# Kernel tuning notes

Hardware: AMD Instinct MI355X
Metric: run time of the kernel (lower is better)

The kernel has to match this reference:

```python
import jax, jax.numpy as jnp
import numpy as np

N_HEADS = 32
N_KV_HEADS = 8
THETA = 10000.0


def _rope_tables(head_dim, seq_len):
    # freqs: [head_dim//2]
    freqs = 1.0 / (THETA ** (jnp.arange(0, head_dim, 2, dtype=jnp.float32) / head_dim))
    ang = jnp.arange(seq_len, dtype=jnp.float32)[:, None] * freqs[None, :]  # [T, hd/2]
    return jnp.cos(ang), jnp.sin(ang)


def _apply_rope(x, cos, sin):
    # x: [B, T, H, hd]; cos/sin: [T, hd/2] -> broadcast [1, T, 1, hd/2]
    x_even = x[..., 0::2]
    x_odd = x[..., 1::2]
    c = cos[None, :, None, :]
    s = sin[None, :, None, :]
    out_even = x_even * c - x_odd * s
    out_odd = x_even * s + x_odd * c
    # interleave back to [..., hd]
    out = jnp.stack([out_even, out_odd], axis=-1)
    return out.reshape(x.shape)


def setup_inputs() -> dict:
    key = jax.random.key(0)
    ks = jax.random.split(key, 5)
    B, T, C = 2, 2048, 2048
    kv_dim = (C // N_HEADS) * N_KV_HEADS  # 512
    sc = 1.0 / np.sqrt(C)
    return {
        "x": jax.random.normal(ks[0], (B, T, C), dtype=jnp.float32),
        "wq": jax.random.normal(ks[1], (C, C), dtype=jnp.float32) * sc,
        "wk": jax.random.normal(ks[2], (C, kv_dim), dtype=jnp.float32) * sc,
        "wv": jax.random.normal(ks[3], (C, kv_dim), dtype=jnp.float32) * sc,
        "wo": jax.random.normal(ks[4], (C, C), dtype=jnp.float32) * sc,
    }


def reference(x, wq, wk, wv, wo):
    B, T, C = x.shape
    hd = C // N_HEADS
    rep = N_HEADS // N_KV_HEADS

    q = (x @ wq).reshape(B, T, N_HEADS, hd)
    k = (x @ wk).reshape(B, T, N_KV_HEADS, hd)
    v = (x @ wv).reshape(B, T, N_KV_HEADS, hd)

    cos, sin = _rope_tables(hd, T)
    q = _apply_rope(q, cos, sin)
    k = _apply_rope(k, cos, sin)

    q = q.transpose(0, 2, 1, 3)  # [B, H, T, hd]
    k = k.transpose(0, 2, 1, 3)  # [B, KV, T, hd]
    v = v.transpose(0, 2, 1, 3)

    # GQA: repeat_interleave kv heads to match q heads
    k = jnp.repeat(k, rep, axis=1)
    v = jnp.repeat(v, rep, axis=1)

    scores = jnp.einsum("bhtd,bhsd->bhts", q, k) / jnp.sqrt(jnp.float32(hd))
    weights = jax.nn.softmax(scores, axis=-1)  # no causal mask, as in source
    out = jnp.einsum("bhts,bhsd->bhtd", weights, v)
    out = out.transpose(0, 2, 1, 3).reshape(B, T, C)
    return out @ wo
```

## Files before the change

kernel.cpp:

```cpp
#include <hip/hip_runtime.h>
#include <hip/hip_bf16.h>


typedef unsigned short u16;
typedef short bf16x8 __attribute__((ext_vector_type(8)));
typedef float f32x4 __attribute__((ext_vector_type(4)));

#define LOG2E 1.4426950408889634f
#define NFREQ (-13.287712379549449f / 32.f)

#if __has_builtin(__builtin_amdgcn_exp2f)
#define EXP2F(x) __builtin_amdgcn_exp2f(x)
#else
#define EXP2F(x) exp2f(x)
#endif

__device__ __forceinline__ float bf2f(u16 u) {
    union { unsigned v; float f; } x; x.v = ((unsigned)u) << 16; return x.f;
}
__device__ __forceinline__ u16 f2bf(float f) {
    unsigned u = __float_as_uint(f);
    u += 0x7fffu + ((u >> 16) & 1u);
    return (u16)(u >> 16);
}
__device__ __forceinline__ unsigned pack_bf16x2(float lo, float hi) {
    unsigned ul = (__float_as_uint(lo) + 0x8000u) >> 16;
    unsigned uh = (__float_as_uint(hi) + 0x8000u) & 0xffff0000u;
    return uh | ul;
}

__device__ __forceinline__ void async_copy16(const void* g, void* l) {
    __builtin_amdgcn_global_load_lds((const __attribute__((address_space(1))) void*)g,
                                     (__attribute__((address_space(3))) void*)l, 16, 0, 0);
}

__global__ void prep_kernel(const float* __restrict__ x,
                            const float* __restrict__ wq, const float* __restrict__ wk,
                            const float* __restrict__ wv, const float* __restrict__ wo,
                            u16* __restrict__ xbf, u16* __restrict__ wqkvT,
                            u16* __restrict__ woT, float2* __restrict__ rtab) {
    const int bz = blockIdx.z;
    if (bz < 4) {
        const int K = 2048;
        const float* W; u16* Wt; int N;
        switch (bz) {
            case 0:  W = wq; Wt = wqkvT;                        N = 2048; break;
            case 1:  W = wk; Wt = wqkvT + (size_t)2048 * 2048;  N = 512;  break;
            case 2:  W = wv; Wt = wqkvT + (size_t)2560 * 2048;  N = 512;  break;
            default: W = wo; Wt = woT;                          N = 2048; break;
        }
        if ((int)blockIdx.x * 32 >= N) return;
        __shared__ float tile[32][33];
        int xx = blockIdx.x * 32 + threadIdx.x;
        int y0 = blockIdx.y * 32 + threadIdx.y;
        #pragma unroll
        for (int r = 0; r < 32; r += 8)
            tile[threadIdx.y + r][threadIdx.x] = W[(size_t)(y0 + r) * N + xx];
        __syncthreads();
        int xo = blockIdx.y * 32 + threadIdx.x;
        int yo0 = blockIdx.x * 32 + threadIdx.y;
        #pragma unroll
        for (int r = 0; r < 32; r += 8)
            Wt[(size_t)(yo0 + r) * K + xo] = f2bf(tile[threadIdx.x][threadIdx.y + r]);
    } else if (bz == 4) {
        int bid = blockIdx.y * gridDim.x + blockIdx.x;
        int tid = threadIdx.y * 32 + threadIdx.x;
        const size_t n4 = (size_t)4096 * 2048 / 4;
        for (size_t i = (size_t)bid * 256 + tid; i < n4; i += (size_t)4096 * 256) {
            float4 v = ((const float4*)x)[i];
            ushort4 o;
            o.x = f2bf(v.x); o.y = f2bf(v.y); o.z = f2bf(v.z); o.w = f2bf(v.w);
            ((ushort4*)xbf)[i] = o;
        }
    } else {
        int bid = blockIdx.y * gridDim.x + blockIdx.x;
        int idx = bid * 256 + threadIdx.y * 32 + threadIdx.x;
        if (idx < 2048 * 32) {
            int t = idx >> 5, i = idx & 31;
            float freq = exp2f((float)i * NFREQ);
            float s, c;
            sincosf((float)t * freq, &s, &c);
            rtab[idx] = make_float2(c, s);
        }
    }
}

__global__ void transpose_perm_kernel(const u16* __restrict__ in, u16* __restrict__ out,
                                      int R, int C) {
    __shared__ u16 tile[32][33];
    int xx = blockIdx.x * 32 + threadIdx.x;
    int y0 = blockIdx.y * 32;
    #pragma unroll
    for (int r = threadIdx.y; r < 32; r += 8)
        tile[r][threadIdx.x] = in[(size_t)(y0 + r) * C + xx];
    __syncthreads();
    int s = y0 + threadIdx.x;
    int c = s & 63;
    int sp = (s & ~63) | (c & 32) | ((c & 15) << 1) | ((c >> 4) & 1);
    int yo = blockIdx.x * 32;
    #pragma unroll
    for (int r = threadIdx.y; r < 32; r += 8)
        out[(size_t)(yo + r) * R + sp] = tile[threadIdx.x][r];
}

__global__ __launch_bounds__(256) void gemm_qkv_kernel(const u16* __restrict__ A,
                                                       const u16* __restrict__ Bt,
                                                       u16* __restrict__ qout,
                                                       u16* __restrict__ kout,
                                                       u16* __restrict__ vout,
                                                       const float2* __restrict__ rope_tab,
                                                       int K) {
    __shared__ __align__(16) u16 As[128 * 64];
    __shared__ __align__(16) u16 Bs[128 * 64];
    const int tid = threadIdx.x;
    const int m0 = blockIdx.y * 128;
    const int n0 = blockIdx.x * 128;
    const int w = tid >> 6, lane = tid & 63;
    const int quad = lane >> 4, ln = lane & 15;
    const int wr = (w >> 1) * 64, wc = (w & 1) * 64;

    f32x4 acc[4][4];
    #pragma unroll
    for (int i = 0; i < 4; i++)
        #pragma unroll
        for (int j = 0; j < 4; j++) acc[i][j] = (f32x4){0.f, 0.f, 0.f, 0.f};

    for (int kt = 0; kt < K; kt += 64) {
        #pragma unroll
        for (int p = 0; p < 4; p++) {
            int chunk = p * 256 + tid;
            int r = chunk >> 3, cl = chunk & 7;
            int cg = cl ^ (r & 7);
            async_copy16(&A[(size_t)(m0 + r) * K + kt + cg * 8], &As[chunk * 8]);
            async_copy16(&Bt[(size_t)(n0 + r) * K + kt + cg * 8], &Bs[chunk * 8]);
        }
        __syncthreads();
        #pragma unroll
        for (int kk = 0; kk < 2; kk++) {
            bf16x8 a[4], b[4];
            #pragma unroll
            for (int i = 0; i < 4; i++) {
                int r = wr + i * 16 + ln;
                int cl = (kk * 4 + quad) ^ (ln & 7);
                a[i] = *(const bf16x8*)(&As[r * 64 + cl * 8]);
            }
            #pragma unroll
            for (int j = 0; j < 4; j++) {
                int r = wc + j * 16 + ln;
                int cl = (kk * 4 + quad) ^ (ln & 7);
                b[j] = *(const bf16x8*)(&Bs[r * 64 + cl * 8]);
            }
            #pragma unroll
            for (int i = 0; i < 4; i++)
                #pragma unroll
                for (int j = 0; j < 4; j++)
                    acc[i][j] = __builtin_amdgcn_mfma_f32_16x16x32_bf16(a[i], b[j], acc[i][j], 0, 0, 0);
        }
        __syncthreads();
    }

    int nb = n0 + wc;
    u16* dst; int ldc, coff; bool isv = false; float scale = 1.f;
    if (nb < 2048)      { dst = qout; ldc = 2048; coff = 0;    scale = 0.125f * LOG2E; }
    else if (nb < 2560) { dst = kout; ldc = 512;  coff = 2048; }
    else                { dst = vout; ldc = 512;  coff = 2560; isv = true; }

    if (isv) {
        #pragma unroll
        for (int i = 0; i < 4; i++)
            #pragma unroll
            for (int r = 0; r < 4; r++) {
                int row = m0 + wr + i * 16 + quad * 4 + r;
                #pragma unroll
                for (int j = 0; j < 4; j++)
                    dst[(size_t)row * ldc + nb + j * 16 + ln - coff] = f2bf(acc[i][j][r]);
            }
    } else {
        float fsin = (ln & 1) ? 1.f : -1.f;
        int fidx[4];
        #pragma unroll
        for (int j = 0; j < 4; j++)
            fidx[j] = ((nb + j * 16 + ln) & 63) >> 1;
        #pragma unroll
        for (int i = 0; i < 4; i++)
            #pragma unroll
            for (int r = 0; r < 4; r++) {
                int row = m0 + wr + i * 16 + quad * 4 + r;
                const float2* trow = rope_tab + (size_t)(row & 2047) * 32;
                #pragma unroll
                for (int j = 0; j < 4; j++) {
                    float v = acc[i][j][r];
                    float p = __shfl_xor(v, 1, 64);
                    float2 cs = trow[fidx[j]];
                    float rr = (v * cs.x + fsin * p * cs.y) * scale;
                    dst[(size_t)row * ldc + nb + j * 16 + ln - coff] = f2bf(rr);
                }
            }
    }
}

__global__ __launch_bounds__(256) void gemm_bt_kernel(const u16* __restrict__ A,
                                                      const u16* __restrict__ Bt,
                                                      float* __restrict__ C,
                                                      int M, int N, int K) {
    __shared__ __align__(16) u16 As[128 * 64];
    __shared__ __align__(16) u16 Bs[128 * 64];
    const int tid = threadIdx.x;
    const int m0 = blockIdx.y * 128;
    const int n0 = blockIdx.x * 128;
    const int w = tid >> 6, lane = tid & 63;
    const int quad = lane >> 4, ln = lane & 15;
    const int wr = (w >> 1) * 64, wc = (w & 1) * 64;

    f32x4 acc[4][4];
    #pragma unroll
    for (int i = 0; i < 4; i++)
        #pragma unroll
        for (int j = 0; j < 4; j++) acc[i][j] = (f32x4){0.f, 0.f, 0.f, 0.f};

    for (int kt = 0; kt < K; kt += 64) {
        #pragma unroll
        for (int p = 0; p < 4; p++) {
            int chunk = p * 256 + tid;
            int r = chunk >> 3, cl = chunk & 7;
            int cg = cl ^ (r & 7);
            async_copy16(&A[(size_t)(m0 + r) * K + kt + cg * 8], &As[chunk * 8]);
            async_copy16(&Bt[(size_t)(n0 + r) * K + kt + cg * 8], &Bs[chunk * 8]);
        }
        __syncthreads();
        #pragma unroll
        for (int kk = 0; kk < 2; kk++) {
            bf16x8 a[4], b[4];
            #pragma unroll
            for (int i = 0; i < 4; i++) {
                int r = wr + i * 16 + ln;
                int cl = (kk * 4 + quad) ^ (ln & 7);
                a[i] = *(const bf16x8*)(&As[r * 64 + cl * 8]);
            }
            #pragma unroll
            for (int j = 0; j < 4; j++) {
                int r = wc + j * 16 + ln;
                int cl = (kk * 4 + quad) ^ (ln & 7);
                b[j] = *(const bf16x8*)(&Bs[r * 64 + cl * 8]);
            }
            #pragma unroll
            for (int i = 0; i < 4; i++)
                #pragma unroll
                for (int j = 0; j < 4; j++)
                    acc[i][j] = __builtin_amdgcn_mfma_f32_16x16x32_bf16(a[i], b[j], acc[i][j], 0, 0, 0);
        }
        __syncthreads();
    }
    #pragma unroll
    for (int i = 0; i < 4; i++)
        #pragma unroll
        for (int r = 0; r < 4; r++) {
            int row = m0 + wr + i * 16 + quad * 4 + r;
            #pragma unroll
            for (int j = 0; j < 4; j++)
                C[(size_t)row * N + n0 + wc + j * 16 + ln] = acc[i][j][r];
        }
}

__global__ __launch_bounds__(256) void attn_kernel(const u16* __restrict__ qb,
                                                   const u16* __restrict__ kb,
                                                   const u16* __restrict__ vtb,
                                                   u16* __restrict__ ob) {
    const int T = 2048;
    const int CQ = 2048, CKV = 512;
    __shared__ __align__(16) u16 Ks[128 * 64];
    __shared__ __align__(16) u16 Vt[64 * 128];
    __shared__ __align__(16) u16 Ps[4 * 32 * 72];

    const int tid = threadIdx.x;
    const int bh = blockIdx.y;
    const int b = bh >> 5, h = bh & 31, kvh = h >> 2;
    const int t0 = blockIdx.x * 128;
    const u16* qbase = qb + ((size_t)(b * T + t0) * CQ + h * 64);
    const u16* kbase = kb + ((size_t)(b * T) * CKV + kvh * 64);
    const u16* vtbase = vtb + ((size_t)(kvh * 64)) * 4096 + b * 2048;

    const int w = tid >> 6, lane = tid & 63, quad = lane >> 4, ln = lane & 15;
    u16* Pw = &Ps[w * 32 * 72];

    bf16x8 ones;
    #pragma unroll
    for (int e = 0; e < 8; e++) ones[e] = (short)0x3F80;

    bf16x8 qf[2][2];
    #pragma unroll
    for (int i = 0; i < 2; i++)
        #pragma unroll
        for (int kk = 0; kk < 2; kk++)
            qf[i][kk] = *(const bf16x8*)(&qbase[(size_t)(w * 32 + i * 16 + ln) * CQ + kk * 32 + quad * 8]);

    f32x4 o_acc[2][4];
    f32x4 l_acc[2];
    #pragma unroll
    for (int i = 0; i < 2; i++) {
        l_acc[i] = (f32x4){0.f, 0.f, 0.f, 0.f};
        #pragma unroll
        for (int j = 0; j < 4; j++) o_acc[i][j] = (f32x4){0.f, 0.f, 0.f, 0.f};
    }

    for (int st = 0; st < T; st += 128) {
        #pragma unroll
        for (int p = 0; p < 4; p++) {
            int chunk = p * 256 + tid;
            int r = chunk >> 3, cl = chunk & 7;
            int cg = cl ^ (r & 7);
            async_copy16(&kbase[(size_t)(st + r) * CKV + cg * 8], &Ks[chunk * 8]);
            int d = chunk >> 4, cl2 = chunk & 15;
            int cg2 = cl2 ^ (d & 7);
            async_copy16(&vtbase[(size_t)d * 4096 + st + cg2 * 8], &Vt[chunk * 8]);
        }
        __syncthreads();

        f32x4 s_acc[2][8];
        #pragma unroll
        for (int i = 0; i < 2; i++)
            #pragma unroll
            for (int j = 0; j < 8; j++) s_acc[i][j] = (f32x4){0.f, 0.f, 0.f, 0.f};
        #pragma unroll
        for (int kk = 0; kk < 2; kk++) {
            bf16x8 bfr[8];
            #pragma unroll
            for (int j = 0; j < 8; j++) {
                int r = j * 16 + ln;
                int cl = (kk * 4 + quad) ^ (ln & 7);
                bfr[j] = *(const bf16x8*)(&Ks[r * 64 + cl * 8]);
            }
            #pragma unroll
            for (int i = 0; i < 2; i++)
                #pragma unroll
                for (int j = 0; j < 8; j++)
                    s_acc[i][j] = __builtin_amdgcn_mfma_f32_16x16x32_bf16(qf[i][kk], bfr[j], s_acc[i][j], 0, 0, 0);
        }

        #pragma unroll
        for (int h2 = 0; h2 < 2; h2++) {
            #pragma unroll
            for (int i = 0; i < 2; i++)
                #pragma unroll
                for (int rr = 0; rr < 4; rr++) {
                    int row = i * 16 + quad * 4 + rr;
                    unsigned* prow = (unsigned*)&Pw[row * 72];
                    float v0 = EXP2F(s_acc[i][h2 * 4 + 0][rr]);
                    float v1 = EXP2F(s_acc[i][h2 * 4 + 1][rr]);
                    float v2 = EXP2F(s_acc[i][h2 * 4 + 2][rr]);
                    float v3 = EXP2F(s_acc[i][h2 * 4 + 3][rr]);
                    prow[ln]      = pack_bf16x2(v0, v1);
                    prow[16 + ln] = pack_bf16x2(v2, v3);
                }
            #pragma unroll
            for (int kk = 0; kk < 2; kk++) {
                bf16x8 pa[2], vb[4];
                #pragma unroll
                for (int i = 0; i < 2; i++)
                    pa[i] = *(const bf16x8*)(&Pw[(i * 16 + ln) * 72 + kk * 32 + quad * 8]);
                #pragma unroll
                for (int jd = 0; jd < 4; jd++) {
                    int d = jd * 16 + ln;
                    int cg = h2 * 8 + kk * 4 + quad;
                    int cl = (cg & 8) | ((cg ^ (d & 7)) & 7);
                    vb[jd] = *(const bf16x8*)(&Vt[d * 128 + cl * 8]);
                }
                #pragma unroll
                for (int i = 0; i < 2; i++) {
                    l_acc[i] = __builtin_amdgcn_mfma_f32_16x16x32_bf16(pa[i], ones, l_acc[i], 0, 0, 0);
                    #pragma unroll
                    for (int jd = 0; jd < 4; jd++)
                        o_acc[i][jd] = __builtin_amdgcn_mfma_f32_16x16x32_bf16(pa[i], vb[jd], o_acc[i][jd], 0, 0, 0);
                }
            }
        }
        __syncthreads();
    }

    #pragma unroll
    for (int i = 0; i < 2; i++)
        #pragma unroll
        for (int rr = 0; rr < 4; rr++) {
            float linv = 1.f / l_acc[i][rr];
            int row = w * 32 + i * 16 + quad * 4 + rr;
            #pragma unroll
            for (int jd = 0; jd < 4; jd++) {
                int col = jd * 16 + ln;
                ob[(size_t)(b * T + t0 + row) * CQ + h * 64 + col] = f2bf(o_acc[i][jd][rr] * linv);
            }
        }
}

#define WS_X_BF   ((size_t)0)
#define WS_WQKVT  ((size_t)16777216)
#define WS_WOT    ((size_t)29360128)
#define WS_QBF    ((size_t)37748736)
#define WS_KBF    ((size_t)54525952)
#define WS_VBF    ((size_t)58720256)
#define WS_ABF    ((size_t)62914560)

extern "C" void kernel_launch(void* const* d_in, const int* in_sizes, int n_in,
                              void* d_out, int out_size, void* d_ws, size_t ws_size,
                              hipStream_t stream) {
    const float* x  = (const float*)d_in[0];
    const float* wq = (const float*)d_in[1];
    const float* wk = (const float*)d_in[2];
    const float* wv = (const float*)d_in[3];
    const float* wo = (const float*)d_in[4];
    char* ws = (char*)d_ws;
    u16* xbf   = (u16*)(ws + WS_X_BF);
    u16* wqkvT = (u16*)(ws + WS_WQKVT);
    u16* woT   = (u16*)(ws + WS_WOT);
    u16* qbf   = (u16*)(ws + WS_QBF);
    u16* kbf   = (u16*)(ws + WS_KBF);
    u16* vbf   = (u16*)(ws + WS_VBF);
    u16* vtbf  = (u16*)(ws + WS_X_BF);
    u16* abf   = (u16*)(ws + WS_ABF);
    float2* rtab = (float2*)(ws + WS_ABF);
    float* out = (float*)d_out;

    prep_kernel<<<dim3(64, 64, 6), dim3(32, 8), 0, stream>>>(x, wq, wk, wv, wo,
                                                             xbf, wqkvT, woT, rtab);

    gemm_qkv_kernel<<<dim3(24, 32), 256, 0, stream>>>(xbf, wqkvT, qbf, kbf, vbf, rtab, 2048);

    transpose_perm_kernel<<<dim3(16, 128), dim3(32, 8), 0, stream>>>(vbf, vtbf, 4096, 512);

    attn_kernel<<<dim3(16, 64), 256, 0, stream>>>(qbf, kbf, vtbf, abf);

    gemm_bt_kernel<<<dim3(16, 32), 256, 0, stream>>>(abf, woT, out, 4096, 2048, 2048);
}
```

Before: 338.4 us.

## Load K and V fragments directly from global memory in attention kernel

Removes the shared-memory staging of K and V tiles and the per-tile barriers. Each wave now reads its MFMA operand fragments straight from global memory (via L1/L2), and the kernel declares a minimum of four blocks per multiprocessor. The aim is to drop LDS traffic and synchronisation and to raise occupancy. In exchange, all four waves load the same K/V data redundantly, and global load latency is exposed without an explicit prefetch.

New measurement: 576.2 us. 70.3% more time.

```diff
diff --git a/kernel.cpp b/kernel.cpp
--- a/kernel.cpp
+++ b/kernel.cpp
@@ -262,14 +262,12 @@
         }
 }
 
-__global__ __launch_bounds__(256) void attn_kernel(const u16* __restrict__ qb,
-                                                   const u16* __restrict__ kb,
-                                                   const u16* __restrict__ vtb,
-                                                   u16* __restrict__ ob) {
+__global__ __launch_bounds__(256, 4) void attn_kernel(const u16* __restrict__ qb,
+                                                      const u16* __restrict__ kb,
+                                                      const u16* __restrict__ vtb,
+                                                      u16* __restrict__ ob) {
     const int T = 2048;
     const int CQ = 2048, CKV = 512;
-    __shared__ __align__(16) u16 Ks[128 * 64];
-    __shared__ __align__(16) u16 Vt[64 * 128];
     __shared__ __align__(16) u16 Ps[4 * 32 * 72];
 
     const int tid = threadIdx.x;
@@ -287,6 +285,9 @@
     #pragma unroll
     for (int e = 0; e < 8; e++) ones[e] = (short)0x3F80;
 
+    const u16* klane = kbase + (size_t)ln * CKV + quad * 8;
+    const u16* vlane = vtbase + (size_t)ln * 4096 + quad * 8;
+
     bf16x8 qf[2][2];
     #pragma unroll
     for (int i = 0; i < 2; i++)
@@ -304,18 +305,6 @@
     }
 
     for (int st = 0; st < T; st += 128) {
-        #pragma unroll
-        for (int p = 0; p < 4; p++) {
-            int chunk = p * 256 + tid;
-            int r = chunk >> 3, cl = chunk & 7;
-            int cg = cl ^ (r & 7);
-            async_copy16(&kbase[(size_t)(st + r) * CKV + cg * 8], &Ks[chunk * 8]);
-            int d = chunk >> 4, cl2 = chunk & 15;
-            int cg2 = cl2 ^ (d & 7);
-            async_copy16(&vtbase[(size_t)d * 4096 + st + cg2 * 8], &Vt[chunk * 8]);
-        }
-        __syncthreads();
-
         f32x4 s_acc[2][8];
         #pragma unroll
         for (int i = 0; i < 2; i++)
@@ -325,11 +314,8 @@
         for (int kk = 0; kk < 2; kk++) {
             bf16x8 bfr[8];
             #pragma unroll
-            for (int j = 0; j < 8; j++) {
-                int r = j * 16 + ln;
-                int cl = (kk * 4 + quad) ^ (ln & 7);
-                bfr[j] = *(const bf16x8*)(&Ks[r * 64 + cl * 8]);
-            }
+            for (int j = 0; j < 8; j++)
+                bfr[j] = *(const bf16x8*)(klane + (size_t)(st + j * 16) * CKV + kk * 32);
             #pragma unroll
             for (int i = 0; i < 2; i++)
                 #pragma unroll
@@ -359,12 +345,8 @@
                 for (int i = 0; i < 2; i++)
                     pa[i] = *(const bf16x8*)(&Pw[(i * 16 + ln) * 72 + kk * 32 + quad * 8]);
                 #pragma unroll
-                for (int jd = 0; jd < 4; jd++) {
-                    int d = jd * 16 + ln;
-                    int cg = h2 * 8 + kk * 4 + quad;
-                    int cl = (cg & 8) | ((cg ^ (d & 7)) & 7);
-                    vb[jd] = *(const bf16x8*)(&Vt[d * 128 + cl * 8]);
-                }
+                for (int jd = 0; jd < 4; jd++)
+                    vb[jd] = *(const bf16x8*)(vlane + (size_t)(jd * 16) * 4096 + st + h2 * 64 + kk * 32);
                 #pragma unroll
                 for (int i = 0; i < 2; i++) {
                     l_acc[i] = __builtin_amdgcn_mfma_f32_16x16x32_bf16(pa[i], ones, l_acc[i], 0, 0, 0);
@@ -374,7 +356,6 @@
                 }
             }
         }
-        __syncthreads();
     }
 
     #pragma unroll
```

## Keep softmax probabilities in registers by computing S^T and permuting V layout

Applied to the files above, without the earlier changes.

The attention kernel now computes the transposed score tile (K as the A operand, Q as B), so each lane's MFMA outputs line up with the A-operand layout needed for the P·V product. The probabilities are packed into bf16x8 fragments straight from registers, and the per-wave shared-memory P buffer with its write/read round trip is removed. To match this, the V transpose kernel uses a new 128-wide column permutation. The change also precomputes the K/V async-copy pointers once and advances them per tile, and wraps the MFMA bursts with s_setprio. The cost is extra register pressure from holding pa[2][4], and correctness depends on the new permutation matching the fragment ordering exactly.

After: 327.9 us. 3.1% less time.

```diff
diff --git a/kernel.cpp b/kernel.cpp
--- a/kernel.cpp
+++ b/kernel.cpp
@@ -5,6 +5,7 @@
 typedef unsigned short u16;
 typedef short bf16x8 __attribute__((ext_vector_type(8)));
 typedef float f32x4 __attribute__((ext_vector_type(4)));
+typedef unsigned uint32x4 __attribute__((ext_vector_type(4)));
 
 #define LOG2E 1.4426950408889634f
 #define NFREQ (-13.287712379549449f / 32.f)
@@ -95,8 +96,8 @@
         tile[r][threadIdx.x] = in[(size_t)(y0 + r) * C + xx];
     __syncthreads();
     int s = y0 + threadIdx.x;
-    int c = s & 63;
-    int sp = (s & ~63) | (c & 32) | ((c & 15) << 1) | ((c >> 4) & 1);
+    int c = s & 127;
+    int sp = (s & ~127) | (c & 96) | ((c & 12) << 1) | ((c & 16) >> 2) | (c & 3);
     int yo = blockIdx.x * 32;
     #pragma unroll
     for (int r = threadIdx.y; r < 32; r += 8)
@@ -270,7 +271,6 @@
     const int CQ = 2048, CKV = 512;
     __shared__ __align__(16) u16 Ks[128 * 64];
     __shared__ __align__(16) u16 Vt[64 * 128];
-    __shared__ __align__(16) u16 Ps[4 * 32 * 72];
 
     const int tid = threadIdx.x;
     const int bh = blockIdx.y;
@@ -281,11 +281,22 @@
     const u16* vtbase = vtb + ((size_t)(kvh * 64)) * 4096 + b * 2048;
 
     const int w = tid >> 6, lane = tid & 63, quad = lane >> 4, ln = lane & 15;
-    u16* Pw = &Ps[w * 32 * 72];
 
     bf16x8 ones;
     #pragma unroll
     for (int e = 0; e < 8; e++) ones[e] = (short)0x3F80;
+
+    const u16* kp[4]; const u16* vp[4];
+    #pragma unroll
+    for (int p = 0; p < 4; p++) {
+        int chunk = p * 256 + tid;
+        int r = chunk >> 3, cl = chunk & 7;
+        int cg = cl ^ (r & 7);
+        kp[p] = kbase + (size_t)r * CKV + cg * 8;
+        int d = chunk >> 4, cl2 = chunk & 15;
+        int cg2 = cl2 ^ (d & 7);
+        vp[p] = vtbase + (size_t)d * 4096 + cg2 * 8;
+    }
 
     bf16x8 qf[2][2];
     #pragma unroll
@@ -307,72 +318,69 @@
         #pragma unroll
         for (int p = 0; p < 4; p++) {
             int chunk = p * 256 + tid;
-            int r = chunk >> 3, cl = chunk & 7;
-            int cg = cl ^ (r & 7);
-            async_copy16(&kbase[(size_t)(st + r) * CKV + cg * 8], &Ks[chunk * 8]);
-            int d = chunk >> 4, cl2 = chunk & 15;
-            int cg2 = cl2 ^ (d & 7);
-            async_copy16(&vtbase[(size_t)d * 4096 + st + cg2 * 8], &Vt[chunk * 8]);
-        }
-        __syncthreads();
-
-        f32x4 s_acc[2][8];
-        #pragma unroll
-        for (int i = 0; i < 2; i++)
-            #pragma unroll
-            for (int j = 0; j < 8; j++) s_acc[i][j] = (f32x4){0.f, 0.f, 0.f, 0.f};
+            async_copy16(kp[p], &Ks[chunk * 8]);
+            async_copy16(vp[p], &Vt[chunk * 8]);
+            kp[p] += 128 * CKV;
+            vp[p] += 128;
+        }
+        __syncthreads();
+
+        f32x4 s_acc[8][2];
+        #pragma unroll
+        for (int j = 0; j < 8; j++)
+            #pragma unroll
+            for (int i = 0; i < 2; i++) s_acc[j][i] = (f32x4){0.f, 0.f, 0.f, 0.f};
         #pragma unroll
         for (int kk = 0; kk < 2; kk++) {
-            bf16x8 bfr[8];
+            bf16x8 kf[8];
             #pragma unroll
             for (int j = 0; j < 8; j++) {
                 int r = j * 16 + ln;
                 int cl = (kk * 4 + quad) ^ (ln & 7);
-                bfr[j] = *(const bf16x8*)(&Ks[r * 64 + cl * 8]);
-            }
-            #pragma unroll
-            for (int i = 0; i < 2; i++)
-                #pragma unroll
-                for (int j = 0; j < 8; j++)
-                    s_acc[i][j] = __builtin_amdgcn_mfma_f32_16x16x32_bf16(qf[i][kk], bfr[j], s_acc[i][j], 0, 0, 0);
-        }
-
-        #pragma unroll
-        for (int h2 = 0; h2 < 2; h2++) {
-            #pragma unroll
-            for (int i = 0; i < 2; i++)
-                #pragma unroll
-                for (int rr = 0; rr < 4; rr++) {
-                    int row = i * 16 + quad * 4 + rr;
-                    unsigned* prow = (unsigned*)&Pw[row * 72];
-                    float v0 = EXP2F(s_acc[i][h2 * 4 + 0][rr]);
-                    float v1 = EXP2F(s_acc[i][h2 * 4 + 1][rr]);
-                    float v2 = EXP2F(s_acc[i][h2 * 4 + 2][rr]);
-                    float v3 = EXP2F(s_acc[i][h2 * 4 + 3][rr]);
-                    prow[ln]      = pack_bf16x2(v0, v1);
-                    prow[16 + ln] = pack_bf16x2(v2, v3);
-                }
-            #pragma unroll
-            for (int kk = 0; kk < 2; kk++) {
-                bf16x8 pa[2], vb[4];
+                kf[j] = *(const bf16x8*)(&Ks[r * 64 + cl * 8]);
+            }
+            __builtin_amdgcn_s_setprio(1);
+            #pragma unroll
+            for (int j = 0; j < 8; j++)
                 #pragma unroll
                 for (int i = 0; i < 2; i++)
-                    pa[i] = *(const bf16x8*)(&Pw[(i * 16 + ln) * 72 + kk * 32 + quad * 8]);
-                #pragma unroll
-                for (int jd = 0; jd < 4; jd++) {
-                    int d = jd * 16 + ln;
-                    int cg = h2 * 8 + kk * 4 + quad;
-                    int cl = (cg & 8) | ((cg ^ (d & 7)) & 7);
-                    vb[jd] = *(const bf16x8*)(&Vt[d * 128 + cl * 8]);
-                }
-                #pragma unroll
-                for (int i = 0; i < 2; i++) {
-                    l_acc[i] = __builtin_amdgcn_mfma_f32_16x16x32_bf16(pa[i], ones, l_acc[i], 0, 0, 0);
-                    #pragma unroll
-                    for (int jd = 0; jd < 4; jd++)
-                        o_acc[i][jd] = __builtin_amdgcn_mfma_f32_16x16x32_bf16(pa[i], vb[jd], o_acc[i][jd], 0, 0, 0);
-                }
-            }
+                    s_acc[j][i] = __builtin_amdgcn_mfma_f32_16x16x32_bf16(kf[j], qf[i][kk], s_acc[j][i], 0, 0, 0);
+            __builtin_amdgcn_s_setprio(0);
+        }
+
+        bf16x8 pa[2][4];
+        #pragma unroll
+        for (int i = 0; i < 2; i++)
+            #pragma unroll
+            for (int c = 0; c < 4; c++) {
+                unsigned w0 = pack_bf16x2(EXP2F(s_acc[2 * c][i][0]),     EXP2F(s_acc[2 * c][i][1]));
+                unsigned w1 = pack_bf16x2(EXP2F(s_acc[2 * c][i][2]),     EXP2F(s_acc[2 * c][i][3]));
+                unsigned w2 = pack_bf16x2(EXP2F(s_acc[2 * c + 1][i][0]), EXP2F(s_acc[2 * c + 1][i][1]));
+                unsigned w3 = pack_bf16x2(EXP2F(s_acc[2 * c + 1][i][2]), EXP2F(s_acc[2 * c + 1][i][3]));
+                union { uint32x4 u; bf16x8 b; } pu;
+                pu.u = (uint32x4){w0, w1, w2, w3};
+                pa[i][c] = pu.b;
+            }
+
+        #pragma unroll
+        for (int c = 0; c < 4; c++) {
+            bf16x8 vb[4];
+            #pragma unroll
+            for (int jd = 0; jd < 4; jd++) {
+                int d = jd * 16 + ln;
+                int cg = c * 4 + quad;
+                int cl = (cg & 8) | ((cg ^ (d & 7)) & 7);
+                vb[jd] = *(const bf16x8*)(&Vt[d * 128 + cl * 8]);
+            }
+            __builtin_amdgcn_s_setprio(1);
+            #pragma unroll
+            for (int i = 0; i < 2; i++) {
+                l_acc[i] = __builtin_amdgcn_mfma_f32_16x16x32_bf16(pa[i][c], ones, l_acc[i], 0, 0, 0);
+                #pragma unroll
+                for (int jd = 0; jd < 4; jd++)
+                    o_acc[i][jd] = __builtin_amdgcn_mfma_f32_16x16x32_bf16(pa[i][c], vb[jd], o_acc[i][jd], 0, 0, 0);
+            }
+            __builtin_amdgcn_s_setprio(0);
         }
         __syncthreads();
     }
```
